# Optimization experiments

Measured on AMD Instinct MI355X. Metric: run time of the kernel, lower is better.

The kernel has to match this reference:

```python
import jax, jax.numpy as jnp
import numpy as np


def setup_inputs() -> dict:
    key = jax.random.key(0)
    ks = jax.random.split(key, 7)
    B, T, I, H, O = 64, 2048, 32, 256, 32
    s = 0.05
    return {
        "x": jax.random.normal(ks[0], (B, T, I), dtype=jnp.float32),
        "W_ih": jax.random.normal(ks[1], (4 * H, I), dtype=jnp.float32) * s,
        "W_hh": jax.random.normal(ks[2], (4 * H, H), dtype=jnp.float32) * s,
        "b_ih": jax.random.normal(ks[3], (4 * H,), dtype=jnp.float32) * s,
        "b_hh": jax.random.normal(ks[4], (4 * H,), dtype=jnp.float32) * s,
        "fc_w": jax.random.normal(ks[5], (O, H), dtype=jnp.float32) * s,
        "fc_b": jax.random.normal(ks[6], (O,), dtype=jnp.float32) * s,
    }


def _lstm(x, W_ih, W_hh, b_ih, b_hh):
    # x: [B,T,I]; PyTorch gate order: i, f, g, o stacked along 4H axis.
    B = x.shape[0]
    H = W_hh.shape[1]
    # Precompute input contributions for all timesteps in one GEMM: [B,T,4H]
    xg = jnp.einsum('bti,gi->btg', x, W_ih) + b_ih + b_hh

    def step(carry, xg_t):
        h, c = carry  # [B,H] each
        gates = xg_t + h @ W_hh.T  # [B,4H]
        i, f, g, o = jnp.split(gates, 4, axis=-1)
        i = jax.nn.sigmoid(i)
        f = jax.nn.sigmoid(f)
        g = jnp.tanh(g)
        o = jax.nn.sigmoid(o)
        c = f * c + i * g
        h = o * jnp.tanh(c)
        return (h, c), h

    h0 = jnp.zeros((B, H), dtype=x.dtype)
    (_, _), hs = jax.lax.scan(step, (h0, h0), jnp.swapaxes(xg, 0, 1))
    return jnp.swapaxes(hs, 0, 1)  # [B,T,H]


def reference(x, W_ih, W_hh, b_ih, b_hh, fc_w, fc_b):
    out = _lstm(x, W_ih, W_hh, b_ih, b_hh)          # [B,T,H]
    # Conv1d(H, O, kernel_size=1) over channel dim == pointwise linear.
    return jnp.einsum('bth,oh->bto', out, fc_w) + fc_b  # [B,T,O]
```

## Files before the change

kernel.cpp:

```cpp
#include <hip/hip_runtime.h>
#include <cstdint>


#define B_  64
#define T_  2048
#define I_  32
#define H_  256
#define G4  1024
#define O_  32

typedef int v16i __attribute__((ext_vector_type(16)));
typedef int v4i  __attribute__((ext_vector_type(4)));
typedef unsigned int v4u __attribute__((ext_vector_type(4)));
typedef _Float16 h2_t __attribute__((ext_vector_type(2)));

#if __has_builtin(__builtin_amdgcn_sdot4)
__device__ __forceinline__ int dot4(int a, int b, int c) {
    return __builtin_amdgcn_sdot4(a, b, c, false);
}
#else
__device__ __forceinline__ int dot4(int a, int b, int c) {
    c += (int)(int8_t)(a)        * (int)(int8_t)(b);
    c += (int)(int8_t)(a >> 8)   * (int)(int8_t)(b >> 8);
    c += (int)(int8_t)(a >> 16)  * (int)(int8_t)(b >> 16);
    c += (int)(int8_t)(a >> 24)  * (int)(int8_t)(b >> 24);
    return c;
}
#endif

__device__ __forceinline__ float fdot2h(h2_t a, h2_t b, float c) {
#if __has_builtin(__builtin_amdgcn_fdot2)
    return __builtin_amdgcn_fdot2(a, b, c, false);
#else
    return c + (float)a[0] * (float)b[0] + (float)a[1] * (float)b[1];
#endif
}

__device__ __forceinline__ float wave64_max_bcast(float v) {
    int t;
    t = __builtin_amdgcn_update_dpp(__float_as_int(v), __float_as_int(v), 0x111, 0xf, 0xf, false);
    v = fmaxf(v, __int_as_float(t));
    t = __builtin_amdgcn_update_dpp(__float_as_int(v), __float_as_int(v), 0x112, 0xf, 0xf, false);
    v = fmaxf(v, __int_as_float(t));
    t = __builtin_amdgcn_update_dpp(__float_as_int(v), __float_as_int(v), 0x114, 0xf, 0xf, false);
    v = fmaxf(v, __int_as_float(t));
    t = __builtin_amdgcn_update_dpp(__float_as_int(v), __float_as_int(v), 0x118, 0xf, 0xf, false);
    v = fmaxf(v, __int_as_float(t));
    t = __builtin_amdgcn_update_dpp(__float_as_int(v), __float_as_int(v), 0x142, 0xa, 0xf, false);
    v = fmaxf(v, __int_as_float(t));
    t = __builtin_amdgcn_update_dpp(__float_as_int(v), __float_as_int(v), 0x143, 0xc, 0xf, false);
    v = fmaxf(v, __int_as_float(t));
    return __int_as_float(__builtin_amdgcn_readlane(__float_as_int(v), 63));
}

__device__ __forceinline__ float halfwave_sum31(float v) {
    int t;
    t = __builtin_amdgcn_update_dpp(0, __float_as_int(v), 0x111, 0xf, 0xf, true); v += __int_as_float(t);
    t = __builtin_amdgcn_update_dpp(0, __float_as_int(v), 0x112, 0xf, 0xf, true); v += __int_as_float(t);
    t = __builtin_amdgcn_update_dpp(0, __float_as_int(v), 0x114, 0xf, 0xf, true); v += __int_as_float(t);
    t = __builtin_amdgcn_update_dpp(0, __float_as_int(v), 0x118, 0xf, 0xf, true); v += __int_as_float(t);
    t = __builtin_amdgcn_update_dpp(0, __float_as_int(v), 0x142, 0xa, 0xf, true); v += __int_as_float(t);
    return v;
}

#define QWHH_OFF 0
#define QWIH_OFF 262144
#define S1_OFF   327680
#define S2_OFF   331776
#define BIAS_OFF 335872
#define XQ_OFF   339968
#define XS_OFF   8728576
#define HBUF_OFF 9252864
#define HREC_STRIDE 320
#define HSLOTS 2049

__device__ __forceinline__ uint32_t pack_q(int q0, int q1, int q2, int q3) {
    return  ((uint32_t)(uint8_t)(int8_t)q0)
          | (((uint32_t)(uint8_t)(int8_t)q1) << 8)
          | (((uint32_t)(uint8_t)(int8_t)q2) << 16)
          | (((uint32_t)(uint8_t)(int8_t)q3) << 24);
}

__device__ __forceinline__ int clamp127(int v) {
    return v < -127 ? -127 : (v > 127 ? 127 : v);
}

__global__ __launch_bounds__(64) void prep_w(
    const float* __restrict__ Whh, const float* __restrict__ Wih,
    const float* __restrict__ bih, const float* __restrict__ bhh,
    uint32_t* __restrict__ qwhh, uint32_t* __restrict__ qwih,
    float* __restrict__ s1, float* __restrict__ s2, float* __restrict__ bias)
{
    const int r = blockIdx.x;
    const int l = threadIdx.x;

    const float4 wv = ((const float4*)(Whh + r * H_))[l];
    float m = fmaxf(fmaxf(fabsf(wv.x), fabsf(wv.y)), fmaxf(fabsf(wv.z), fabsf(wv.w)));
    #pragma unroll
    for (int s = 1; s < 64; s <<= 1) m = fmaxf(m, __shfl_xor(m, s, 64));
    const float S1 = fmaxf(m, 1e-20f) / 127.f;

    float xm = (l < I_) ? fabsf(Wih[r * I_ + l]) : 0.f;
    #pragma unroll
    for (int s = 1; s < 64; s <<= 1) xm = fmaxf(xm, __shfl_xor(xm, s, 64));
    const float S2 = fmaxf(xm, 1e-20f) / 127.f;

    {
        const float r1 = 1.f / S1;
        qwhh[l * G4 + r] = pack_q(
            clamp127((int)rintf(wv.x * r1)), clamp127((int)rintf(wv.y * r1)),
            clamp127((int)rintf(wv.z * r1)), clamp127((int)rintf(wv.w * r1)));
    }
    if (l < 8) {
        const float4 xw = ((const float4*)(Wih + r * I_))[l];
        const float r2 = 1.f / S2;
        qwih[l * G4 + r] = pack_q(
            clamp127((int)rintf(xw.x * r2)), clamp127((int)rintf(xw.y * r2)),
            clamp127((int)rintf(xw.z * r2)), clamp127((int)rintf(xw.w * r2)));
    } else if (l < 16) {
        const int j = l - 8;
        const float4 xw = ((const float4*)(Wih + r * I_))[j];
        const float r2 = 1.f / S2;
        float v0 = xw.x * r2, v1 = xw.y * r2, v2 = xw.z * r2, v3 = xw.w * r2;
        int a0 = clamp127((int)rintf(v0)), a1 = clamp127((int)rintf(v1));
        int a2 = clamp127((int)rintf(v2)), a3 = clamp127((int)rintf(v3));
        qwih[(8 + j) * G4 + r] = pack_q(
            clamp127((int)rintf((v0 - (float)a0) * 127.f)),
            clamp127((int)rintf((v1 - (float)a1) * 127.f)),
            clamp127((int)rintf((v2 - (float)a2) * 127.f)),
            clamp127((int)rintf((v3 - (float)a3) * 127.f)));
    }
    if (l == 0) { s1[r] = S1; s2[r] = S2; bias[r] = bih[r] + bhh[r]; }
}

__global__ __launch_bounds__(256) void prep_x(
    const float* __restrict__ x, uint32_t* __restrict__ xq, float* __restrict__ xs)
{
    __shared__ float xb[64 * 32];
    const int base = blockIdx.x * 64 * 32;
    for (int i = threadIdx.x; i < 2048; i += 256) xb[i] = x[base + i];
    __syncthreads();
    const int t = threadIdx.x;
    if (t < 64) {
        float m = 0.f;
        for (int k = 0; k < 32; k++) m = fmaxf(m, fabsf(xb[t * 32 + k]));
        const float S = fmaxf(m, 1e-20f) / 127.f;
        const int row = blockIdx.x * 64 + t;
        xs[row] = S;
        const float rS = 1.f / S;
        for (int j = 0; j < 8; j++) {
            int qa[4], qb[4];
            for (int e = 0; e < 4; e++) {
                float v = xb[t * 32 + j * 4 + e] * rS;
                int a = clamp127((int)rintf(v));
                int b = clamp127((int)rintf((v - (float)a) * 127.f));
                qa[e] = a; qb[e] = b;
            }
            xq[row * 16 + j]     = pack_q(qa[0], qa[1], qa[2], qa[3]);
            xq[row * 16 + 8 + j] = pack_q(qb[0], qb[1], qb[2], qb[3]);
        }
    }
}

__device__ __forceinline__ float xdots(v4u x0, v4u x1, v4u x2, v4u x3, float sx,
                                       const uint32_t* wA, const uint32_t* wB,
                                       float S2, float bias_r) {
    int aA = 0, aM = 0;
    #pragma unroll
    for (int j = 0; j < 4; j++) {
        aA = dot4((int)wA[j],     (int)x0[j], aA);
        aM = dot4((int)wA[j],     (int)x2[j], aM);
        aM = dot4((int)wB[j],     (int)x0[j], aM);
        aA = dot4((int)wA[4 + j], (int)x1[j], aA);
        aM = dot4((int)wA[4 + j], (int)x3[j], aM);
        aM = dot4((int)wB[4 + j], (int)x1[j], aM);
    }
    return ((float)aA + (float)aM * (1.f / 127.f)) * (S2 * sx) + bias_r;
}

__global__ __launch_bounds__(1024, 4) void lstm_main(
    const uint32_t* __restrict__ qwhh, const uint32_t* __restrict__ qwih,
    const float* __restrict__ s1v, const float* __restrict__ s2v,
    const float* __restrict__ biasv,
    const uint32_t* __restrict__ xq, const float* __restrict__ xs,
    const float* __restrict__ fcw, const float* __restrict__ fcb,
    char* __restrict__ hbuf, float* __restrict__ out)
{
    const int b   = blockIdx.x;
    const int tid = threadIdx.x;

    __shared__ float    gbuf[768];
    __shared__ uint32_t hf16[128];

    uint32_t w[64], wA[8], wB[8];
    #pragma unroll
    for (int d = 0; d < 64; d++) w[d] = qwhh[d * G4 + tid];
    #pragma unroll
    for (int j = 0; j < 8; j++) { wA[j] = qwih[j * G4 + tid]; wB[j] = qwih[(8 + j) * G4 + tid]; }
    const float S1 = s1v[tid], S2 = s2v[tid], bias_r = biasv[tid];

    const int o_ = tid >> 5, kc = tid & 31;
    h2_t fw[4];
    {
        const float* fr = fcw + o_ * H_ + kc * 8;
        #pragma unroll
        for (int j = 0; j < 4; j++) {
            h2_t p; p[0] = (_Float16)fr[2 * j]; p[1] = (_Float16)fr[2 * j + 1];
            fw[j] = p;
        }
    }
    const float fcb_v = fcb[o_];

    char* hb = hbuf + (size_t)b * (HSLOTS * HREC_STRIDE);
    if (tid < H_) hb[2048 * HREC_STRIDE + tid] = 0;
    if (tid >= 256 && tid < 260) ((float*)(hb + 2048 * HREC_STRIDE + 256))[tid - 256] = 0.f;

    const uint32_t* xqb  = xq + (size_t)(b * T_) * 16;
    const float*    xsb  = xs + (size_t)(b * T_);
    float*          outb = out + (size_t)(b * T_) * O_;

    float c_state = 0.f;
    float x_part;
    {
        const v4u x0 = *(const v4u*)(xqb);     const v4u x1 = *(const v4u*)(xqb + 4);
        const v4u x2 = *(const v4u*)(xqb + 8); const v4u x3 = *(const v4u*)(xqb + 12);
        x_part = xdots(x0, x1, x2, x3, xsb[0], wA, wB, S2, bias_r);
    }

    __syncthreads();

    for (int t = 0; t < T_; t++) {
        const uint32_t slot = (t == 0) ? 2048u : ((uint32_t)(t * 1993) & 2047u);
        const char* hrec = hb + (size_t)slot * HREC_STRIDE;
        v16i h0, h1, h2, h3; v4i scv;
        asm volatile("s_load_dwordx16 %0, %5, 0x0\n\t"
                     "s_load_dwordx16 %1, %5, 0x40\n\t"
                     "s_load_dwordx16 %2, %5, 0x80\n\t"
                     "s_load_dwordx16 %3, %5, 0xc0\n\t"
                     "s_load_dwordx4  %4, %5, 0x100"
                     : "=&s"(h0), "=&s"(h1), "=&s"(h2), "=&s"(h3), "=&s"(scv)
                     : "s"(hrec)
                     : "memory");

        const int tn = (t + 1 < T_) ? (t + 1) : t;
        const uint32_t* px = xqb + (size_t)tn * 16;
        const v4u x0 = *(const v4u*)(px);     const v4u x1 = *(const v4u*)(px + 4);
        const v4u x2 = *(const v4u*)(px + 8); const v4u x3 = *(const v4u*)(px + 12);
        const float sx = xsb[tn];

        if (t > 0) {
            const v4u hv = *(const v4u*)(&hf16[4 * kc]);
            union { uint32_t u; h2_t h; } u0, u1, u2, u3;
            u0.u = hv[0]; u1.u = hv[1]; u2.u = hv[2]; u3.u = hv[3];
            float acc = 0.f;
            acc = fdot2h(fw[0], u0.h, acc);
            acc = fdot2h(fw[1], u1.h, acc);
            acc = fdot2h(fw[2], u2.h, acc);
            acc = fdot2h(fw[3], u3.h, acc);
            acc = halfwave_sum31(acc);
            if ((tid & 31) == 31) outb[(t - 1) * O_ + o_] = acc + fcb_v;
        }

        asm volatile("s_waitcnt lgkmcnt(0)"
                     : "+s"(h0), "+s"(h1), "+s"(h2), "+s"(h3), "+s"(scv)
                     :
                     : "memory");

        int a0 = 0, a1 = 0, a2 = 0, a3 = 0;
        #pragma unroll
        for (int d = 0; d < 16; d++) {
            a0 = dot4((int)w[d],      h0[d], a0);
            a1 = dot4((int)w[16 + d], h1[d], a1);
            a2 = dot4((int)w[32 + d], h2[d], a2);
            a3 = dot4((int)w[48 + d], h3[d], a3);
        }
        const float hsum = (float)a0 * __int_as_float(scv[0])
                         + (float)a1 * __int_as_float(scv[1])
                         + (float)a2 * __int_as_float(scv[2])
                         + (float)a3 * __int_as_float(scv[3]);
        const float gate = hsum * S1 + x_part;

        if (tid >= 256) gbuf[tid - 256] = gate;
        __syncthreads();

        const uint32_t wslot = (uint32_t)((t + 1) * 1993) & 2047u;
        char* hw = hb + (size_t)wslot * HREC_STRIDE;
        if (tid < H_) {
            const float gi = gate;
            const float gf = gbuf[tid];
            const float gg = gbuf[256 + tid];
            const float go = gbuf[512 + tid];
            const float i_ = 1.f / (1.f + __expf(-gi));
            const float f_ = 1.f / (1.f + __expf(-gf));
            const float g_ = 2.f / (1.f + __expf(-2.f * gg)) - 1.f;
            const float oo = 1.f / (1.f + __expf(-go));
            c_state = f_ * c_state + i_ * g_;
            const float tc = 2.f / (1.f + __expf(-2.f * c_state)) - 1.f;
            const float hval = oo * tc;
            ((_Float16*)hf16)[tid] = (_Float16)hval;

            float m = wave64_max_bcast(fabsf(hval));
            m = fmaxf(m, 1e-12f);
            const float rq = 127.f / m;
            const int q = clamp127((int)rintf(hval * rq));
            hw[tid] = (char)(int8_t)q;
            if ((tid & 63) == 0)
                ((float*)(hw + 256))[tid >> 6] = m * (1.f / 127.f);
        }

        x_part = xdots(x0, x1, x2, x3, sx, wA, wB, S2, bias_r);

        __syncthreads();
    }

    {
        const v4u hv = *(const v4u*)(&hf16[4 * kc]);
        union { uint32_t u; h2_t h; } u0, u1, u2, u3;
        u0.u = hv[0]; u1.u = hv[1]; u2.u = hv[2]; u3.u = hv[3];
        float acc = 0.f;
        acc = fdot2h(fw[0], u0.h, acc);
        acc = fdot2h(fw[1], u1.h, acc);
        acc = fdot2h(fw[2], u2.h, acc);
        acc = fdot2h(fw[3], u3.h, acc);
        acc = halfwave_sum31(acc);
        if ((tid & 31) == 31) outb[(T_ - 1) * O_ + o_] = acc + fcb_v;
    }
}

extern "C" void kernel_launch(void* const* d_in, const int* in_sizes, int n_in,
                              void* d_out, int out_size, void* d_ws, size_t ws_size,
                              hipStream_t stream) {
    const float* x    = (const float*)d_in[0];
    const float* Wih  = (const float*)d_in[1];
    const float* Whh  = (const float*)d_in[2];
    const float* bih  = (const float*)d_in[3];
    const float* bhh  = (const float*)d_in[4];
    const float* fcw  = (const float*)d_in[5];
    const float* fcb  = (const float*)d_in[6];
    float* out = (float*)d_out;

    char* ws = (char*)d_ws;
    uint32_t* qwhh = (uint32_t*)(ws + QWHH_OFF);
    uint32_t* qwih = (uint32_t*)(ws + QWIH_OFF);
    float*    s1   = (float*)(ws + S1_OFF);
    float*    s2   = (float*)(ws + S2_OFF);
    float*    bias = (float*)(ws + BIAS_OFF);
    uint32_t* xq   = (uint32_t*)(ws + XQ_OFF);
    float*    xs   = (float*)(ws + XS_OFF);
    char*     hbuf = ws + HBUF_OFF;

    prep_w<<<G4, 64, 0, stream>>>(Whh, Wih, bih, bhh, qwhh, qwih, s1, s2, bias);
    prep_x<<<(B_ * T_) / 64, 256, 0, stream>>>(x, xq, xs);
    lstm_main<<<B_, 1024, 0, stream>>>(qwhh, qwih, s1, s2, bias, xq, xs,
                                       fcw, fcb, hbuf, out);
}
```

Baseline: 3.711 ms.

## Restructure LSTM recurrence to 256 threads each owning all four gates

The main kernel now runs 256 threads per batch row instead of 1024. Each thread holds the int8 W_hh rows for all four gates of one hidden unit in registers, so the cross-thread gate exchange and one of the two barriers per step go away. The hidden state moves from a global scratch buffer read through scalar loads to a double-buffered LDS buffer. The input projection switches from two-level int8 quantization to fp16 dot2, and the FC output uses 8-lane reductions. Each thread now does four times the dot products and needs far more registers, and only 4 waves per block are available to hide latency.

```diff
diff --git a/kernel.cpp b/kernel.cpp
--- a/kernel.cpp
+++ b/kernel.cpp
@@ -6,11 +6,8 @@
 #define T_  2048
 #define I_  32
 #define H_  256
-#define G4  1024
 #define O_  32
 
-typedef int v16i __attribute__((ext_vector_type(16)));
-typedef int v4i  __attribute__((ext_vector_type(4)));
 typedef unsigned int v4u __attribute__((ext_vector_type(4)));
 typedef _Float16 h2_t __attribute__((ext_vector_type(2)));
 
@@ -53,26 +50,19 @@
     return __int_as_float(__builtin_amdgcn_readlane(__float_as_int(v), 63));
 }
 
-__device__ __forceinline__ float halfwave_sum31(float v) {
+__device__ __forceinline__ float sum8(float v) {
     int t;
     t = __builtin_amdgcn_update_dpp(0, __float_as_int(v), 0x111, 0xf, 0xf, true); v += __int_as_float(t);
     t = __builtin_amdgcn_update_dpp(0, __float_as_int(v), 0x112, 0xf, 0xf, true); v += __int_as_float(t);
     t = __builtin_amdgcn_update_dpp(0, __float_as_int(v), 0x114, 0xf, 0xf, true); v += __int_as_float(t);
-    t = __builtin_amdgcn_update_dpp(0, __float_as_int(v), 0x118, 0xf, 0xf, true); v += __int_as_float(t);
-    t = __builtin_amdgcn_update_dpp(0, __float_as_int(v), 0x142, 0xa, 0xf, true); v += __int_as_float(t);
     return v;
 }
 
-#define QWHH_OFF 0
-#define QWIH_OFF 262144
+#define QW_OFF   0
+#define WIH_OFF  262144
 #define S1_OFF   327680
-#define S2_OFF   331776
-#define BIAS_OFF 335872
-#define XQ_OFF   339968
-#define XS_OFF   8728576
-#define HBUF_OFF 9252864
-#define HREC_STRIDE 320
-#define HSLOTS 2049
+#define BIAS_OFF 331776
+#define XH_OFF   335872
 
 __device__ __forceinline__ uint32_t pack_q(int q0, int q1, int q2, int q3) {
     return  ((uint32_t)(uint8_t)(int8_t)q0)
@@ -88,242 +78,197 @@
 __global__ __launch_bounds__(64) void prep_w(
     const float* __restrict__ Whh, const float* __restrict__ Wih,
     const float* __restrict__ bih, const float* __restrict__ bhh,
-    uint32_t* __restrict__ qwhh, uint32_t* __restrict__ qwih,
-    float* __restrict__ s1, float* __restrict__ s2, float* __restrict__ bias)
+    uint32_t* __restrict__ qw4, uint32_t* __restrict__ wih4,
+    float* __restrict__ s1v, float* __restrict__ biasv)
 {
-    const int r = blockIdx.x;
-    const int l = threadIdx.x;
-
-    const float4 wv = ((const float4*)(Whh + r * H_))[l];
+    const int gr = blockIdx.x;
+    const int c  = threadIdx.x;
+    const int j  = gr >> 8;
+    const int r  = gr & 255;
+
+    const float4 wv = ((const float4*)(Whh + gr * H_))[c];
     float m = fmaxf(fmaxf(fabsf(wv.x), fabsf(wv.y)), fmaxf(fabsf(wv.z), fabsf(wv.w)));
     #pragma unroll
     for (int s = 1; s < 64; s <<= 1) m = fmaxf(m, __shfl_xor(m, s, 64));
     const float S1 = fmaxf(m, 1e-20f) / 127.f;
-
-    float xm = (l < I_) ? fabsf(Wih[r * I_ + l]) : 0.f;
-    #pragma unroll
-    for (int s = 1; s < 64; s <<= 1) xm = fmaxf(xm, __shfl_xor(xm, s, 64));
-    const float S2 = fmaxf(xm, 1e-20f) / 127.f;
+    const float r1 = 1.f / S1;
 
     {
-        const float r1 = 1.f / S1;
-        qwhh[l * G4 + r] = pack_q(
+        const int d = j * 64 + c;
+        qw4[(d >> 2) * 1024 + r * 4 + (d & 3)] = pack_q(
             clamp127((int)rintf(wv.x * r1)), clamp127((int)rintf(wv.y * r1)),
             clamp127((int)rintf(wv.z * r1)), clamp127((int)rintf(wv.w * r1)));
     }
-    if (l < 8) {
-        const float4 xw = ((const float4*)(Wih + r * I_))[l];
-        const float r2 = 1.f / S2;
-        qwih[l * G4 + r] = pack_q(
-            clamp127((int)rintf(xw.x * r2)), clamp127((int)rintf(xw.y * r2)),
-            clamp127((int)rintf(xw.z * r2)), clamp127((int)rintf(xw.w * r2)));
-    } else if (l < 16) {
-        const int j = l - 8;
-        const float4 xw = ((const float4*)(Wih + r * I_))[j];
-        const float r2 = 1.f / S2;
-        float v0 = xw.x * r2, v1 = xw.y * r2, v2 = xw.z * r2, v3 = xw.w * r2;
-        int a0 = clamp127((int)rintf(v0)), a1 = clamp127((int)rintf(v1));
-        int a2 = clamp127((int)rintf(v2)), a3 = clamp127((int)rintf(v3));
-        qwih[(8 + j) * G4 + r] = pack_q(
-            clamp127((int)rintf((v0 - (float)a0) * 127.f)),
-            clamp127((int)rintf((v1 - (float)a1) * 127.f)),
-            clamp127((int)rintf((v2 - (float)a2) * 127.f)),
-            clamp127((int)rintf((v3 - (float)a3) * 127.f)));
-    }
-    if (l == 0) { s1[r] = S1; s2[r] = S2; bias[r] = bih[r] + bhh[r]; }
-}
-
-__global__ __launch_bounds__(256) void prep_x(
-    const float* __restrict__ x, uint32_t* __restrict__ xq, float* __restrict__ xs)
+    if (c < 16) {
+        union { uint32_t u; h2_t h; } z;
+        z.h[0] = (_Float16)Wih[gr * I_ + 2 * c];
+        z.h[1] = (_Float16)Wih[gr * I_ + 2 * c + 1];
+        const int dd = j * 16 + c;
+        wih4[(dd >> 2) * 1024 + r * 4 + (dd & 3)] = z.u;
+    }
+    if (c == 0) { s1v[gr] = S1; biasv[gr] = bih[gr] + bhh[gr]; }
+}
+
+__global__ __launch_bounds__(256) void prep_xh(
+    const float* __restrict__ x, uint32_t* __restrict__ xh)
 {
-    __shared__ float xb[64 * 32];
-    const int base = blockIdx.x * 64 * 32;
-    for (int i = threadIdx.x; i < 2048; i += 256) xb[i] = x[base + i];
+    const int i = blockIdx.x * 256 + threadIdx.x;
+    const float2 v = ((const float2*)x)[i];
+    union { uint32_t u; h2_t h; } z;
+    z.h[0] = (_Float16)v.x; z.h[1] = (_Float16)v.y;
+    xh[i] = z.u;
+}
+
+__global__ __launch_bounds__(256, 1) void lstm_main(
+    const uint32_t* __restrict__ qw4, const uint32_t* __restrict__ wih4,
+    const float* __restrict__ s1v, const float* __restrict__ biasv,
+    const uint32_t* __restrict__ xh, const float* __restrict__ fcw,
+    const float* __restrict__ fcb, float* __restrict__ out)
+{
+    const int b  = blockIdx.x;
+    const int r  = threadIdx.x;
+    const int ln = r & 63;
+    const int wv = r >> 6;
+
+    __shared__ uint32_t hqb[2][64];
+    __shared__ __align__(16) float hscb[2][4];
+    __shared__ uint32_t hfb[2][128];
+
+    v4u w4[64];
+    #pragma unroll
+    for (int d4 = 0; d4 < 64; d4++) w4[d4] = ((const v4u*)qw4)[d4 * 256 + r];
+    v4u wx[16];
+    #pragma unroll
+    for (int d4 = 0; d4 < 16; d4++) wx[d4] = ((const v4u*)wih4)[d4 * 256 + r];
+    float S1j[4], bj[4];
+    #pragma unroll
+    for (int j = 0; j < 4; j++) { S1j[j] = s1v[j * 256 + r]; bj[j] = biasv[j * 256 + r]; }
+
+    const int o_ = r >> 3, ks = r & 7;
+    h2_t fw[16];
+    {
+        const float* fr = fcw + o_ * H_ + ks * 32;
+        #pragma unroll
+        for (int i = 0; i < 16; i++) {
+            h2_t p; p[0] = (_Float16)fr[2 * i]; p[1] = (_Float16)fr[2 * i + 1];
+            fw[i] = p;
+        }
+    }
+    const float fcb_v = fcb[o_];
+
+    if (r < 4) hscb[1][r] = 0.f;
     __syncthreads();
-    const int t = threadIdx.x;
-    if (t < 64) {
-        float m = 0.f;
-        for (int k = 0; k < 32; k++) m = fmaxf(m, fabsf(xb[t * 32 + k]));
-        const float S = fmaxf(m, 1e-20f) / 127.f;
-        const int row = blockIdx.x * 64 + t;
-        xs[row] = S;
-        const float rS = 1.f / S;
-        for (int j = 0; j < 8; j++) {
-            int qa[4], qb[4];
-            for (int e = 0; e < 4; e++) {
-                float v = xb[t * 32 + j * 4 + e] * rS;
-                int a = clamp127((int)rintf(v));
-                int b = clamp127((int)rintf((v - (float)a) * 127.f));
-                qa[e] = a; qb[e] = b;
+
+    const uint32_t* xb   = xh + (size_t)(b * T_) * 16;
+    float*          outb = out + (size_t)(b * T_) * O_;
+
+    float c_state = 0.f;
+
+    for (int t = 0; t < T_; t++) {
+        const int pb = (t & 1) ^ 1, cb = t & 1;
+
+        const v4u* xv = (const v4u*)(xb + (size_t)t * 16);
+        const v4u x0 = xv[0], x1 = xv[1], x2 = xv[2], x3 = xv[3];
+
+        const v4u*   hqv = (const v4u*)&hqb[pb][0];
+        const float4 scv = *(const float4*)&hscb[pb][0];
+        const float  scar[4] = { scv.x, scv.y, scv.z, scv.w };
+
+        float a0 = 0.f, a1 = 0.f, a2 = 0.f, a3 = 0.f;
+        #pragma unroll
+        for (int g = 0; g < 4; g++) {
+            v4u hg[4];
+            #pragma unroll
+            for (int q = 0; q < 4; q++) hg[q] = hqv[g * 4 + q];
+            int i0 = 0, i1 = 0, i2 = 0, i3 = 0;
+            #pragma unroll
+            for (int q = 0; q < 4; q++) {
+                #pragma unroll
+                for (int e = 0; e < 4; e++) {
+                    const int hv = (int)hg[q][e];
+                    i0 = dot4((int)w4[ 0 + g * 4 + q][e], hv, i0);
+                    i1 = dot4((int)w4[16 + g * 4 + q][e], hv, i1);
+                    i2 = dot4((int)w4[32 + g * 4 + q][e], hv, i2);
+                    i3 = dot4((int)w4[48 + g * 4 + q][e], hv, i3);
+                }
             }
-            xq[row * 16 + j]     = pack_q(qa[0], qa[1], qa[2], qa[3]);
-            xq[row * 16 + 8 + j] = pack_q(qb[0], qb[1], qb[2], qb[3]);
-        }
-    }
-}
-
-__device__ __forceinline__ float xdots(v4u x0, v4u x1, v4u x2, v4u x3, float sx,
-                                       const uint32_t* wA, const uint32_t* wB,
-                                       float S2, float bias_r) {
-    int aA = 0, aM = 0;
-    #pragma unroll
-    for (int j = 0; j < 4; j++) {
-        aA = dot4((int)wA[j],     (int)x0[j], aA);
-        aM = dot4((int)wA[j],     (int)x2[j], aM);
-        aM = dot4((int)wB[j],     (int)x0[j], aM);
-        aA = dot4((int)wA[4 + j], (int)x1[j], aA);
-        aM = dot4((int)wA[4 + j], (int)x3[j], aM);
-        aM = dot4((int)wB[4 + j], (int)x1[j], aM);
-    }
-    return ((float)aA + (float)aM * (1.f / 127.f)) * (S2 * sx) + bias_r;
-}
-
-__global__ __launch_bounds__(1024, 4) void lstm_main(
-    const uint32_t* __restrict__ qwhh, const uint32_t* __restrict__ qwih,
-    const float* __restrict__ s1v, const float* __restrict__ s2v,
-    const float* __restrict__ biasv,
-    const uint32_t* __restrict__ xq, const float* __restrict__ xs,
-    const float* __restrict__ fcw, const float* __restrict__ fcb,
-    char* __restrict__ hbuf, float* __restrict__ out)
-{
-    const int b   = blockIdx.x;
-    const int tid = threadIdx.x;
-
-    __shared__ float    gbuf[768];
-    __shared__ uint32_t hf16[128];
-
-    uint32_t w[64], wA[8], wB[8];
-    #pragma unroll
-    for (int d = 0; d < 64; d++) w[d] = qwhh[d * G4 + tid];
-    #pragma unroll
-    for (int j = 0; j < 8; j++) { wA[j] = qwih[j * G4 + tid]; wB[j] = qwih[(8 + j) * G4 + tid]; }
-    const float S1 = s1v[tid], S2 = s2v[tid], bias_r = biasv[tid];
-
-    const int o_ = tid >> 5, kc = tid & 31;
-    h2_t fw[4];
+            a0 = fmaf((float)i0, scar[g], a0);
+            a1 = fmaf((float)i1, scar[g], a1);
+            a2 = fmaf((float)i2, scar[g], a2);
+            a3 = fmaf((float)i3, scar[g], a3);
+        }
+
+        if (t > 0) {
+            const v4u* hfv = (const v4u*)&hfb[pb][0];
+            v4u fh[4];
+            #pragma unroll
+            for (int i = 0; i < 4; i++) fh[i] = hfv[ks * 4 + i];
+            float acc = 0.f;
+            #pragma unroll
+            for (int i = 0; i < 16; i++) {
+                union { uint32_t u; h2_t h; } z;
+                z.u = fh[i >> 2][i & 3];
+                acc = fdot2h(fw[i], z.h, acc);
+            }
+            acc = sum8(acc);
+            if (ks == 7) outb[(t - 1) * O_ + o_] = acc + fcb_v;
+        }
+
+        float xd0 = 0.f, xd1 = 0.f, xd2 = 0.f, xd3 = 0.f;
+        {
+            const v4u xg4[4] = { x0, x1, x2, x3 };
+            #pragma unroll
+            for (int d4 = 0; d4 < 4; d4++) {
+                #pragma unroll
+                for (int e = 0; e < 4; e++) {
+                    union { uint32_t u; h2_t h; } zx, z0, z1, z2, z3;
+                    zx.u = xg4[d4][e];
+                    z0.u = wx[ 0 + d4][e]; xd0 = fdot2h(z0.h, zx.h, xd0);
+                    z1.u = wx[ 4 + d4][e]; xd1 = fdot2h(z1.h, zx.h, xd1);
+                    z2.u = wx[ 8 + d4][e]; xd2 = fdot2h(z2.h, zx.h, xd2);
+                    z3.u = wx[12 + d4][e]; xd3 = fdot2h(z3.h, zx.h, xd3);
+                }
+            }
+        }
+
+        const float g0 = fmaf(a0, S1j[0], xd0 + bj[0]);
+        const float g1 = fmaf(a1, S1j[1], xd1 + bj[1]);
+        const float g2 = fmaf(a2, S1j[2], xd2 + bj[2]);
+        const float g3 = fmaf(a3, S1j[3], xd3 + bj[3]);
+        const float i_ = 1.f / (1.f + __expf(-g0));
+        const float f_ = 1.f / (1.f + __expf(-g1));
+        const float gg = 2.f / (1.f + __expf(-2.f * g2)) - 1.f;
+        const float oo = 1.f / (1.f + __expf(-g3));
+        c_state = f_ * c_state + i_ * gg;
+        const float tc = 2.f / (1.f + __expf(-2.f * c_state)) - 1.f;
+        const float hval = oo * tc;
+
+        float m = wave64_max_bcast(fabsf(hval));
+        m = fmaxf(m, 1e-12f);
+        const int q = clamp127((int)rintf(hval * (127.f / m)));
+        ((char*)&hqb[cb][0])[r] = (char)(int8_t)q;
+        if (ln == 0) hscb[cb][wv] = m * (1.f / 127.f);
+        ((_Float16*)&hfb[cb][0])[r] = (_Float16)hval;
+
+        asm volatile("s_waitcnt lgkmcnt(0)" ::: "memory");
+        __builtin_amdgcn_s_barrier();
+    }
+
     {
-        const float* fr = fcw + o_ * H_ + kc * 8;
-        #pragma unroll
-        for (int j = 0; j < 4; j++) {
-            h2_t p; p[0] = (_Float16)fr[2 * j]; p[1] = (_Float16)fr[2 * j + 1];
-            fw[j] = p;
-        }
-    }
-    const float fcb_v = fcb[o_];
-
-    char* hb = hbuf + (size_t)b * (HSLOTS * HREC_STRIDE);
-    if (tid < H_) hb[2048 * HREC_STRIDE + tid] = 0;
-    if (tid >= 256 && tid < 260) ((float*)(hb + 2048 * HREC_STRIDE + 256))[tid - 256] = 0.f;
-
-    const uint32_t* xqb  = xq + (size_t)(b * T_) * 16;
-    const float*    xsb  = xs + (size_t)(b * T_);
-    float*          outb = out + (size_t)(b * T_) * O_;
-
-    float c_state = 0.f;
-    float x_part;
-    {
-        const v4u x0 = *(const v4u*)(xqb);     const v4u x1 = *(const v4u*)(xqb + 4);
-        const v4u x2 = *(const v4u*)(xqb + 8); const v4u x3 = *(const v4u*)(xqb + 12);
-        x_part = xdots(x0, x1, x2, x3, xsb[0], wA, wB, S2, bias_r);
-    }
-
-    __syncthreads();
-
-    for (int t = 0; t < T_; t++) {
-        const uint32_t slot = (t == 0) ? 2048u : ((uint32_t)(t * 1993) & 2047u);
-        const char* hrec = hb + (size_t)slot * HREC_STRIDE;
-        v16i h0, h1, h2, h3; v4i scv;
-        asm volatile("s_load_dwordx16 %0, %5, 0x0\n\t"
-                     "s_load_dwordx16 %1, %5, 0x40\n\t"
-                     "s_load_dwordx16 %2, %5, 0x80\n\t"
-                     "s_load_dwordx16 %3, %5, 0xc0\n\t"
-                     "s_load_dwordx4  %4, %5, 0x100"
-                     : "=&s"(h0), "=&s"(h1), "=&s"(h2), "=&s"(h3), "=&s"(scv)
-                     : "s"(hrec)
-                     : "memory");
-
-        const int tn = (t + 1 < T_) ? (t + 1) : t;
-        const uint32_t* px = xqb + (size_t)tn * 16;
-        const v4u x0 = *(const v4u*)(px);     const v4u x1 = *(const v4u*)(px + 4);
-        const v4u x2 = *(const v4u*)(px + 8); const v4u x3 = *(const v4u*)(px + 12);
-        const float sx = xsb[tn];
-
-        if (t > 0) {
-            const v4u hv = *(const v4u*)(&hf16[4 * kc]);
-            union { uint32_t u; h2_t h; } u0, u1, u2, u3;
-            u0.u = hv[0]; u1.u = hv[1]; u2.u = hv[2]; u3.u = hv[3];
-            float acc = 0.f;
-            acc = fdot2h(fw[0], u0.h, acc);
-            acc = fdot2h(fw[1], u1.h, acc);
-            acc = fdot2h(fw[2], u2.h, acc);
-            acc = fdot2h(fw[3], u3.h, acc);
-            acc = halfwave_sum31(acc);
-            if ((tid & 31) == 31) outb[(t - 1) * O_ + o_] = acc + fcb_v;
-        }
-
-        asm volatile("s_waitcnt lgkmcnt(0)"
-                     : "+s"(h0), "+s"(h1), "+s"(h2), "+s"(h3), "+s"(scv)
-                     :
-                     : "memory");
-
-        int a0 = 0, a1 = 0, a2 = 0, a3 = 0;
-        #pragma unroll
-        for (int d = 0; d < 16; d++) {
-            a0 = dot4((int)w[d],      h0[d], a0);
-            a1 = dot4((int)w[16 + d], h1[d], a1);
-            a2 = dot4((int)w[32 + d], h2[d], a2);
-            a3 = dot4((int)w[48 + d], h3[d], a3);
-        }
-        const float hsum = (float)a0 * __int_as_float(scv[0])
-                         + (float)a1 * __int_as_float(scv[1])
-                         + (float)a2 * __int_as_float(scv[2])
-                         + (float)a3 * __int_as_float(scv[3]);
-        const float gate = hsum * S1 + x_part;
-
-        if (tid >= 256) gbuf[tid - 256] = gate;
-        __syncthreads();
-
-        const uint32_t wslot = (uint32_t)((t + 1) * 1993) & 2047u;
-        char* hw = hb + (size_t)wslot * HREC_STRIDE;
-        if (tid < H_) {
-            const float gi = gate;
-            const float gf = gbuf[tid];
-            const float gg = gbuf[256 + tid];
-            const float go = gbuf[512 + tid];
-            const float i_ = 1.f / (1.f + __expf(-gi));
-            const float f_ = 1.f / (1.f + __expf(-gf));
-            const float g_ = 2.f / (1.f + __expf(-2.f * gg)) - 1.f;
-            const float oo = 1.f / (1.f + __expf(-go));
-            c_state = f_ * c_state + i_ * g_;
-            const float tc = 2.f / (1.f + __expf(-2.f * c_state)) - 1.f;
-            const float hval = oo * tc;
-            ((_Float16*)hf16)[tid] = (_Float16)hval;
-
-            float m = wave64_max_bcast(fabsf(hval));
-            m = fmaxf(m, 1e-12f);
-            const float rq = 127.f / m;
-            const int q = clamp127((int)rintf(hval * rq));
-            hw[tid] = (char)(int8_t)q;
-            if ((tid & 63) == 0)
-                ((float*)(hw + 256))[tid >> 6] = m * (1.f / 127.f);
-        }
-
-        x_part = xdots(x0, x1, x2, x3, sx, wA, wB, S2, bias_r);
-
-        __syncthreads();
-    }
-
-    {
-        const v4u hv = *(const v4u*)(&hf16[4 * kc]);
-        union { uint32_t u; h2_t h; } u0, u1, u2, u3;
-        u0.u = hv[0]; u1.u = hv[1]; u2.u = hv[2]; u3.u = hv[3];
+        const int pb = (T_ - 1) & 1;
+        const v4u* hfv = (const v4u*)&hfb[pb][0];
+        v4u fh[4];
+        #pragma unroll
+        for (int i = 0; i < 4; i++) fh[i] = hfv[ks * 4 + i];
         float acc = 0.f;
-        acc = fdot2h(fw[0], u0.h, acc);
-        acc = fdot2h(fw[1], u1.h, acc);
-        acc = fdot2h(fw[2], u2.h, acc);
-        acc = fdot2h(fw[3], u3.h, acc);
-        acc = halfwave_sum31(acc);
-        if ((tid & 31) == 31) outb[(T_ - 1) * O_ + o_] = acc + fcb_v;
+        #pragma unroll
+        for (int i = 0; i < 16; i++) {
+            union { uint32_t u; h2_t h; } z;
+            z.u = fh[i >> 2][i & 3];
+            acc = fdot2h(fw[i], z.h, acc);
+        }
+        acc = sum8(acc);
+        if (ks == 7) outb[(T_ - 1) * O_ + o_] = acc + fcb_v;
     }
 }
 
@@ -340,17 +285,13 @@
     float* out = (float*)d_out;
 
     char* ws = (char*)d_ws;
-    uint32_t* qwhh = (uint32_t*)(ws + QWHH_OFF);
-    uint32_t* qwih = (uint32_t*)(ws + QWIH_OFF);
-    float*    s1   = (float*)(ws + S1_OFF);
-    float*    s2   = (float*)(ws + S2_OFF);
-    float*    bias = (float*)(ws + BIAS_OFF);
-    uint32_t* xq   = (uint32_t*)(ws + XQ_OFF);
-    float*    xs   = (float*)(ws + XS_OFF);
-    char*     hbuf = ws + HBUF_OFF;
-
-    prep_w<<<G4, 64, 0, stream>>>(Whh, Wih, bih, bhh, qwhh, qwih, s1, s2, bias);
-    prep_x<<<(B_ * T_) / 64, 256, 0, stream>>>(x, xq, xs);
-    lstm_main<<<B_, 1024, 0, stream>>>(qwhh, qwih, s1, s2, bias, xq, xs,
-                                       fcw, fcb, hbuf, out);
-}
+    uint32_t* qw4   = (uint32_t*)(ws + QW_OFF);
+    uint32_t* wih4  = (uint32_t*)(ws + WIH_OFF);
+    float*    s1v   = (float*)(ws + S1_OFF);
+    float*    biasv = (float*)(ws + BIAS_OFF);
+    uint32_t* xh    = (uint32_t*)(ws + XH_OFF);
+
+    prep_w<<<1024, 64, 0, stream>>>(Whh, Wih, bih, bhh, qw4, wih4, s1v, biasv);
+    prep_xh<<<(B_ * T_ * 16) / 256, 256, 0, stream>>>(x, xh);
+    lstm_main<<<B_, 256, 0, stream>>>(qw4, wih4, s1v, biasv, xh, fcw, fcb, out);
+}
```

Result: faster. 3.410 ms (-8.1%).
